# Kernel optimization log

Hardware: AMD Instinct MI355X
Metric: run time of the kernel (lower is better)

Reference implementation:

```python
import jax, jax.numpy as jnp
import numpy as np

B, H, L, D, S = 4, 16, 4096, 64, 128

def setup_inputs() -> dict:
    key = jax.random.key(0)
    k1, k2 = jax.random.split(key)
    x = jax.random.normal(k1, (B, H, L, D), dtype=jnp.float32)
    c = jax.random.normal(k2, (H, S, D), dtype=jnp.float32)
    # codebook rows are unit-normalized at init (matches torch init)
    c = c / jnp.linalg.norm(c, axis=-1, keepdims=True)
    return {"x": x, "c": c}

def reference(x, c):
    # cosine-similarity scores: [B,H,L,S]
    cos_sim = jnp.einsum('bhld,hsd->bhls', x, c)
    delta_index = jnp.argmax(cos_sim, axis=-1)            # [B,H,L]
    delta_onehot = jax.nn.one_hot(delta_index, c.shape[-2], dtype=jnp.float32)  # [B,H,L,S]
    return (delta_onehot, c)
```

## Files before the change

kernel.cpp:

```cpp
#include <hip/hip_runtime.h>
#include <math.h>

constexpr int BB = 4;
constexpr int HH = 16;
constexpr int LL = 4096;
constexpr int DD = 64;
constexpr int SS = 128;
constexpr int BM = 128;

constexpr float TAU = 2e-3f;

typedef __attribute__((ext_vector_type(8))) short bf16x8;
typedef __attribute__((ext_vector_type(4))) float f32x4;

#define MFMA16 __builtin_amdgcn_mfma_f32_16x16x32_bf16

__device__ __forceinline__ unsigned short f2bf(float v) {
    unsigned u = __float_as_uint(v);
    return (unsigned short)((u + 0x7fffu + ((u >> 16) & 1u)) >> 16);
}
__device__ __forceinline__ float bf2f(unsigned short b) {
    return __uint_as_float(((unsigned)b) << 16);
}
__device__ __forceinline__ unsigned swz(unsigned a) {
    return a ^ (((a >> 8) & 3u) << 5);
}
__device__ __forceinline__ void st8(unsigned char* s, unsigned a, uint2 d) {
    *(uint2*)(s + swz(a)) = d;
}
__device__ __forceinline__ bf16x8 ld8(const unsigned char* s, unsigned a) {
    return *(const bf16x8*)(s + swz(a));
}

__global__ __launch_bounds__(256) void quantizer_kernel(
    const float* __restrict__ x,
    const float* __restrict__ c,
    float* __restrict__ out,
    float* __restrict__ out_c)
{
    __shared__ __align__(16) unsigned char smem[65536];
    __shared__ int amax[BM];
    __shared__ int s_nflag;
    __shared__ int s_flag[BM];
    __shared__ float s_fsc[SS];

    const int tid = threadIdx.x;
    const int blk = blockIdx.x;
    const long long r0 = (long long)blk * BM;
    const int h = (int)((r0 >> 12) & (HH - 1));
    const float* __restrict__ chead = c + (size_t)h * SS * DD;

    if (tid == 0) s_nflag = 0;

    {
        const float4* __restrict__ xg = (const float4*)(x + (size_t)r0 * DD);
        const float4* __restrict__ cg = (const float4*)chead;
        #pragma unroll
        for (int it = 0; it < 8; ++it) {
            const int idx = it * 256 + tid;
            const int d4  = idx & 15;
            const int row = idx >> 4;
            const int kt  = d4 >> 3;
            const int lsl = ((((d4 & 7) >> 1) << 4) | (row & 15));
            const int boff = (d4 & 1) * 8;
            const int t8  = row >> 4;
            const unsigned bhi =
                (unsigned)((((kt << 3) | t8) << 10) + lsl * 16 + boff);
            const unsigned blo = bhi + (16u << 10);
            {
                float4 v = xg[idx];
                unsigned short h0 = f2bf(v.x), h1 = f2bf(v.y),
                               h2 = f2bf(v.z), h3 = f2bf(v.w);
                unsigned short l0 = f2bf(v.x - bf2f(h0)),
                               l1 = f2bf(v.y - bf2f(h1)),
                               l2 = f2bf(v.z - bf2f(h2)),
                               l3 = f2bf(v.w - bf2f(h3));
                st8(smem, bhi, make_uint2((unsigned)h0 | ((unsigned)h1 << 16),
                                          (unsigned)h2 | ((unsigned)h3 << 16)));
                st8(smem, blo, make_uint2((unsigned)l0 | ((unsigned)l1 << 16),
                                          (unsigned)l2 | ((unsigned)l3 << 16)));
            }
            {
                float4 v = cg[idx];
                unsigned short h0 = f2bf(v.x), h1 = f2bf(v.y),
                               h2 = f2bf(v.z), h3 = f2bf(v.w);
                unsigned short l0 = f2bf(v.x - bf2f(h0)),
                               l1 = f2bf(v.y - bf2f(h1)),
                               l2 = f2bf(v.z - bf2f(h2)),
                               l3 = f2bf(v.w - bf2f(h3));
                st8(smem, 32768u + bhi,
                    make_uint2((unsigned)h0 | ((unsigned)h1 << 16),
                               (unsigned)h2 | ((unsigned)h3 << 16)));
                st8(smem, 32768u + blo,
                    make_uint2((unsigned)l0 | ((unsigned)l1 << 16),
                               (unsigned)l2 | ((unsigned)l3 << 16)));
            }
        }
    }
    __syncthreads();

    const int wv = tid >> 6;
    const int lane = tid & 63;
    const int ln15 = lane & 15;

    bf16x8 af[2][2][2];
    #pragma unroll
    for (int rtb = 0; rtb < 2; ++rtb)
        #pragma unroll
        for (int kt = 0; kt < 2; ++kt)
            #pragma unroll
            for (int sp = 0; sp < 2; ++sp)
                af[rtb][kt][sp] = ld8(smem,
                    (unsigned)((((sp << 4) | (kt << 3) | (2 * wv + rtb)) << 10)
                               + lane * 16));

    float m1[2][4], m2[2][4];
    int   mi_[2][4];
    #pragma unroll
    for (int rtb = 0; rtb < 2; ++rtb)
        #pragma unroll
        for (int r = 0; r < 4; ++r) {
            m1[rtb][r] = -INFINITY; m2[rtb][r] = -INFINITY; mi_[rtb][r] = 0;
        }

    #pragma unroll
    for (int ct = 0; ct < 8; ++ct) {
        const unsigned bb = 32768u + (unsigned)(ct << 10) + (unsigned)(lane * 16);
        bf16x8 b10 = ld8(smem, bb);
        bf16x8 b11 = ld8(smem, bb + (1u << 13));
        bf16x8 b20 = ld8(smem, bb + (1u << 14));
        bf16x8 b21 = ld8(smem, bb + (1u << 14) + (1u << 13));
        #pragma unroll
        for (int rtb = 0; rtb < 2; ++rtb) {
            f32x4 acc = {0.f, 0.f, 0.f, 0.f};
            acc = MFMA16(af[rtb][0][1], b10, acc, 0, 0, 0);
            acc = MFMA16(af[rtb][1][1], b11, acc, 0, 0, 0);
            acc = MFMA16(af[rtb][0][0], b20, acc, 0, 0, 0);
            acc = MFMA16(af[rtb][1][0], b21, acc, 0, 0, 0);
            acc = MFMA16(af[rtb][0][0], b10, acc, 0, 0, 0);
            acc = MFMA16(af[rtb][1][0], b11, acc, 0, 0, 0);
            #pragma unroll
            for (int r = 0; r < 4; ++r) {
                const float v = acc[r];
                const int col = ct * 16 + ln15;
                if (v > m1[rtb][r]) {
                    m2[rtb][r] = m1[rtb][r]; m1[rtb][r] = v; mi_[rtb][r] = col;
                } else {
                    m2[rtb][r] = fmaxf(m2[rtb][r], v);
                }
            }
        }
    }

    #pragma unroll
    for (int rtb = 0; rtb < 2; ++rtb) {
        #pragma unroll
        for (int r = 0; r < 4; ++r) {
            float a1 = m1[rtb][r], a2 = m2[rtb][r];
            int ai = mi_[rtb][r];
            #pragma unroll
            for (int off = 1; off <= 8; off <<= 1) {
                const float o1 = __shfl_xor(a1, off);
                const float o2 = __shfl_xor(a2, off);
                const int   oi = __shfl_xor(ai, off);
                const bool take = (o1 > a1) || (o1 == a1 && oi < ai);
                const float n2 = take ? fmaxf(a1, o2) : fmaxf(a2, o1);
                if (take) { a1 = o1; ai = oi; }
                a2 = n2;
            }
            if (ln15 == 0) {
                const int row = (2 * wv + rtb) * 16 + (lane >> 4) * 4 + r;
                if (a1 - a2 >= TAU) {
                    amax[row] = ai;
                } else {
                    const int p = atomicAdd(&s_nflag, 1);
                    s_flag[p] = row;
                }
            }
        }
    }
    __syncthreads();

    const int nf = s_nflag;
    for (int f = 0; f < nf; ++f) {
        const int row = s_flag[f];
        if (tid < SS) {
            const float4* __restrict__ xr =
                (const float4*)(x + (size_t)(r0 + row) * DD);
            const float4* __restrict__ cr =
                (const float4*)(chead + (size_t)tid * DD);
            float sc = 0.f;
            #pragma unroll
            for (int q = 0; q < 16; ++q) {
                const float4 a = xr[q];
                const float4 b = cr[q];
                sc = fmaf(a.x, b.x, sc); sc = fmaf(a.y, b.y, sc);
                sc = fmaf(a.z, b.z, sc); sc = fmaf(a.w, b.w, sc);
            }
            s_fsc[tid] = sc;
        }
        __syncthreads();
        if (tid == 0) {
            float bv = s_fsc[0]; int bi = 0;
            for (int s = 1; s < SS; ++s)
                if (s_fsc[s] > bv) { bv = s_fsc[s]; bi = s; }
            amax[row] = bi;
        }
        __syncthreads();
    }

    float4* __restrict__ op = (float4*)(out + (size_t)r0 * SS);
    #pragma unroll 4
    for (int i = tid; i < BM * (SS / 4); i += 256) {
        const int rr = i >> 5;
        const int s0 = (i & 31) * 4;
        const int am = amax[rr];
        float4 v;
        v.x = (s0 + 0 == am) ? 1.f : 0.f;
        v.y = (s0 + 1 == am) ? 1.f : 0.f;
        v.z = (s0 + 2 == am) ? 1.f : 0.f;
        v.w = (s0 + 3 == am) ? 1.f : 0.f;
        op[i] = v;
    }

    if (blk < 128) {
        const float4* __restrict__ src = (const float4*)c;
        float4* __restrict__ dst = (float4*)out_c;
        const int idx = blk * 256 + tid;
        dst[idx] = src[idx];
    }
}

extern "C" void kernel_launch(void* const* d_in, const int* in_sizes, int n_in,
                              void* d_out, int out_size, void* d_ws, size_t ws_size,
                              hipStream_t stream) {
    const float* x = (const float*)d_in[0];
    const float* c = (const float*)d_in[1];
    float* out = (float*)d_out;
    float* out_c = out + (size_t)BB * HH * LL * SS;

    const int rows = BB * HH * LL;
    const int blocks = rows / BM;
    quantizer_kernel<<<blocks, 256, 0, stream>>>(x, c, out, out_c);
}
```

Before: 216.1 us.

## Precompute split-bf16 codebook in workspace and load x fragments directly to registers

A small pre-kernel converts each head's codebook into hi/lo bf16 MFMA fragment layout in workspace. The main kernel then copies it into LDS with global_load_lds instead of converting it in every block. x rows are now loaded straight from global memory into register fragments, with no trip through shared memory. LDS use drops from 64KB to 32KB, which may allow higher occupancy, and the hi part is now taken by truncation. The cost is an extra kernel launch, and the direct x loads are less coalesced.

```diff
diff --git a/kernel.cpp b/kernel.cpp
--- a/kernel.cpp
+++ b/kernel.cpp
@@ -19,32 +19,65 @@
     unsigned u = __float_as_uint(v);
     return (unsigned short)((u + 0x7fffu + ((u >> 16) & 1u)) >> 16);
 }
-__device__ __forceinline__ float bf2f(unsigned short b) {
-    return __uint_as_float(((unsigned)b) << 16);
-}
-__device__ __forceinline__ unsigned swz(unsigned a) {
-    return a ^ (((a >> 8) & 3u) << 5);
-}
-__device__ __forceinline__ void st8(unsigned char* s, unsigned a, uint2 d) {
-    *(uint2*)(s + swz(a)) = d;
-}
-__device__ __forceinline__ bf16x8 ld8(const unsigned char* s, unsigned a) {
-    return *(const bf16x8*)(s + swz(a));
-}
-
+
+__device__ __forceinline__ void split8(const float4 va, const float4 vb,
+                                       uint4* hi, uint4* lo) {
+    const float v[8] = {va.x, va.y, va.z, va.w, vb.x, vb.y, vb.z, vb.w};
+    unsigned hw[4], lw[4];
+    #pragma unroll
+    for (int p = 0; p < 4; ++p) {
+        const unsigned u0 = __float_as_uint(v[2 * p]);
+        const unsigned u1 = __float_as_uint(v[2 * p + 1]);
+        const unsigned h0 = u0 & 0xffff0000u;
+        const unsigned h1 = u1 & 0xffff0000u;
+        hw[p] = (u0 >> 16) | h1;
+        lw[p] = (unsigned)f2bf(v[2 * p] - __uint_as_float(h0))
+              | ((unsigned)f2bf(v[2 * p + 1] - __uint_as_float(h1)) << 16);
+    }
+    *hi = make_uint4(hw[0], hw[1], hw[2], hw[3]);
+    *lo = make_uint4(lw[0], lw[1], lw[2], lw[3]);
+}
+
+union FragU { uint4 q; bf16x8 v; };
+
+__global__ __launch_bounds__(256) void convert_c_kernel(
+    const float* __restrict__ c, unsigned char* __restrict__ ws)
+{
+    const int sid = blockIdx.x * 256 + threadIdx.x;
+    const int h  = sid >> 10;
+    const int r  = sid & 1023;
+    const int kt = r >> 9;
+    const int ct = (r >> 6) & 7;
+    const int ln = r & 63;
+    const int cc = ct * 16 + (ln & 15);
+    const int k0 = kt * 32 + (ln >> 4) * 8;
+    const float4* src = (const float4*)(c + ((size_t)h * SS + cc) * DD + k0);
+    uint4 hi, lo;
+    split8(src[0], src[1], &hi, &lo);
+    unsigned char* base =
+        ws + (size_t)h * 32768 + (size_t)(((kt << 3) | ct) * 1024 + ln * 16);
+    *(uint4*)(base) = hi;
+    *(uint4*)(base + 16384) = lo;
+}
+
+template <bool USE_WS>
 __global__ __launch_bounds__(256) void quantizer_kernel(
     const float* __restrict__ x,
     const float* __restrict__ c,
+    const unsigned char* __restrict__ ws,
     float* __restrict__ out,
     float* __restrict__ out_c)
 {
-    __shared__ __align__(16) unsigned char smem[65536];
+    __shared__ __align__(16) unsigned char smemB[32768];
     __shared__ int amax[BM];
     __shared__ int s_nflag;
     __shared__ int s_flag[BM];
     __shared__ float s_fsc[SS];
 
     const int tid = threadIdx.x;
+    const int wv = tid >> 6;
+    const int lane = tid & 63;
+    const int ln15 = lane & 15;
     const int blk = blockIdx.x;
     const long long r0 = (long long)blk * BM;
     const int h = (int)((r0 >> 12) & (HH - 1));
@@ -52,67 +85,50 @@
 
     if (tid == 0) s_nflag = 0;
 
-    {
-        const float4* __restrict__ xg = (const float4*)(x + (size_t)r0 * DD);
-        const float4* __restrict__ cg = (const float4*)chead;
+    if (USE_WS) {
+        const unsigned char* wsb = ws + (size_t)h * 32768;
         #pragma unroll
         for (int it = 0; it < 8; ++it) {
-            const int idx = it * 256 + tid;
-            const int d4  = idx & 15;
-            const int row = idx >> 4;
-            const int kt  = d4 >> 3;
-            const int lsl = ((((d4 & 7) >> 1) << 4) | (row & 15));
-            const int boff = (d4 & 1) * 8;
-            const int t8  = row >> 4;
-            const unsigned bhi =
-                (unsigned)((((kt << 3) | t8) << 10) + lsl * 16 + boff);
-            const unsigned blo = bhi + (16u << 10);
-            {
-                float4 v = xg[idx];
-                unsigned short h0 = f2bf(v.x), h1 = f2bf(v.y),
-                               h2 = f2bf(v.z), h3 = f2bf(v.w);
-                unsigned short l0 = f2bf(v.x - bf2f(h0)),
-                               l1 = f2bf(v.y - bf2f(h1)),
-                               l2 = f2bf(v.z - bf2f(h2)),
-                               l3 = f2bf(v.w - bf2f(h3));
-                st8(smem, bhi, make_uint2((unsigned)h0 | ((unsigned)h1 << 16),
-                                          (unsigned)h2 | ((unsigned)h3 << 16)));
-                st8(smem, blo, make_uint2((unsigned)l0 | ((unsigned)l1 << 16),
-                                          (unsigned)l2 | ((unsigned)l3 << 16)));
-            }
-            {
-                float4 v = cg[idx];
-                unsigned short h0 = f2bf(v.x), h1 = f2bf(v.y),
-                               h2 = f2bf(v.z), h3 = f2bf(v.w);
-                unsigned short l0 = f2bf(v.x - bf2f(h0)),
-                               l1 = f2bf(v.y - bf2f(h1)),
-                               l2 = f2bf(v.z - bf2f(h2)),
-                               l3 = f2bf(v.w - bf2f(h3));
-                st8(smem, 32768u + bhi,
-                    make_uint2((unsigned)h0 | ((unsigned)h1 << 16),
-                               (unsigned)h2 | ((unsigned)h3 << 16)));
-                st8(smem, 32768u + blo,
-                    make_uint2((unsigned)l0 | ((unsigned)l1 << 16),
-                               (unsigned)l2 | ((unsigned)l3 << 16)));
-            }
+            const unsigned off = (unsigned)(wv * 8192 + it * 1024);
+            __builtin_amdgcn_global_load_lds(
+                (const __attribute__((address_space(1))) unsigned*)
+                    (wsb + off + (unsigned)(lane * 16)),
+                (__attribute__((address_space(3))) unsigned*)(smemB + off),
+                16, 0, 0);
+        }
+    } else {
+        #pragma unroll
+        for (int it = 0; it < 4; ++it) {
+            const int sid = it * 256 + tid;
+            const int kt = sid >> 9;
+            const int ct = (sid >> 6) & 7;
+            const int ln = sid & 63;
+            const int cc = ct * 16 + (ln & 15);
+            const int k0 = kt * 32 + (ln >> 4) * 8;
+            const float4* src = (const float4*)(chead + (size_t)cc * DD + k0);
+            uint4 hi, lo;
+            split8(src[0], src[1], &hi, &lo);
+            unsigned char* dst = smemB + ((kt << 3) | ct) * 1024 + ln * 16;
+            *(uint4*)dst = hi;
+            *(uint4*)(dst + 16384) = lo;
+        }
+    }
+
+    bf16x8 af[2][2][2];
+    #pragma unroll
+    for (int rtb = 0; rtb < 2; ++rtb) {
+        const size_t row = (size_t)(r0 + wv * 32 + rtb * 16 + ln15);
+        const float* xr = x + row * DD + (lane >> 4) * 8;
+        #pragma unroll
+        for (int kt = 0; kt < 2; ++kt) {
+            const float4* s4 = (const float4*)(xr + kt * 32);
+            FragU hi, lo;
+            split8(s4[0], s4[1], &hi.q, &lo.q);
+            af[rtb][kt][0] = hi.v;
+            af[rtb][kt][1] = lo.v;
         }
     }
     __syncthreads();
-
-    const int wv = tid >> 6;
-    const int lane = tid & 63;
-    const int ln15 = lane & 15;
-
-    bf16x8 af[2][2][2];
-    #pragma unroll
-    for (int rtb = 0; rtb < 2; ++rtb)
-        #pragma unroll
-        for (int kt = 0; kt < 2; ++kt)
-            #pragma unroll
-            for (int sp = 0; sp < 2; ++sp)
-                af[rtb][kt][sp] = ld8(smem,
-                    (unsigned)((((sp << 4) | (kt << 3) | (2 * wv + rtb)) << 10)
-                               + lane * 16));
 
     float m1[2][4], m2[2][4];
     int   mi_[2][4];
@@ -125,11 +141,11 @@
 
     #pragma unroll
     for (int ct = 0; ct < 8; ++ct) {
-        const unsigned bb = 32768u + (unsigned)(ct << 10) + (unsigned)(lane * 16);
-        bf16x8 b10 = ld8(smem, bb);
-        bf16x8 b11 = ld8(smem, bb + (1u << 13));
-        bf16x8 b20 = ld8(smem, bb + (1u << 14));
-        bf16x8 b21 = ld8(smem, bb + (1u << 14) + (1u << 13));
+        const unsigned bb = (unsigned)(ct << 10) + (unsigned)(lane * 16);
+        const bf16x8 b10 = *(const bf16x8*)(smemB + bb);
+        const bf16x8 b11 = *(const bf16x8*)(smemB + bb + 8192);
+        const bf16x8 b20 = *(const bf16x8*)(smemB + bb + 16384);
+        const bf16x8 b21 = *(const bf16x8*)(smemB + bb + 24576);
         #pragma unroll
         for (int rtb = 0; rtb < 2; ++rtb) {
             f32x4 acc = {0.f, 0.f, 0.f, 0.f};
@@ -241,5 +257,14 @@
 
     const int rows = BB * HH * LL;
     const int blocks = rows / BM;
-    quantizer_kernel<<<blocks, 256, 0, stream>>>(x, c, out, out_c);
-}
+    const size_t ws_need = (size_t)HH * 32768;
+
+    if (d_ws != nullptr && ws_size >= ws_need) {
+        convert_c_kernel<<<64, 256, 0, stream>>>(c, (unsigned char*)d_ws);
+        quantizer_kernel<true><<<blocks, 256, 0, stream>>>(
+            x, c, (const unsigned char*)d_ws, out, out_c);
+    } else {
+        quantizer_kernel<false><<<blocks, 256, 0, stream>>>(
+            x, c, nullptr, out, out_c);
+    }
+}
```

After: 202.9 us. 1.07x faster.
